# Optimization experiments

Measured on AMD Instinct MI355X. Metric: run time of the kernel, lower is better.

Reference implementation:

```python
import jax, jax.numpy as jnp
import numpy as np

TEMP = 0.05  # Trainer temp


def setup_inputs() -> dict:
    key = jax.random.key(0)
    k1, k2, k3 = jax.random.split(key, 3)
    B, C, D = 4096, 32768, 256
    x = jax.random.normal(k1, (B, D), dtype=jnp.float32)
    centrals = jax.random.normal(k2, (C, D), dtype=jnp.float32)
    # memory bank rows are kept unit-norm by the update rule
    centrals = centrals / jnp.linalg.norm(centrals, axis=1, keepdims=True)
    labels = jax.random.randint(k3, (B,), 0, C)
    return {"x": x, "centrals": centrals, "labels": labels}


def reference(x, centrals, labels):
    # new_f = F.normalize(model_out, dim=1)
    f = x / jnp.linalg.norm(x, axis=1, keepdims=True)          # [B, D]
    # CM.forward: inputs.mm(features.t()), then /= temp
    logits = (f @ centrals.T) / TEMP                           # [B, C]
    # ups = gather(exp(logits), labels); down = sum(exp(logits));  ups/down == softmax prob at label
    logp = jax.nn.log_softmax(logits, axis=1)
    p = jnp.exp(jnp.take_along_axis(logp, labels[:, None], axis=1)[:, 0])  # [B]
    return p
```

## Files before the change

kernel.cpp:

```cpp
#include <hip/hip_runtime.h>
#include <stdint.h>

typedef int i32x4 __attribute__((ext_vector_type(4)));
typedef int i32x8 __attribute__((ext_vector_type(8)));
typedef float f32x4 __attribute__((ext_vector_type(4)));

#define B_ROWS 4096
#define C_COLS 32768
#define D_DIM 256
#define LOG2E_OVER_TEMP 28.853900817779268f

#define BM 256
#define BC 128
#define CSPLIT 64
#define CPB (C_COLS / CSPLIT)
#define CTILES (CPB / BC)
#define NWAVES 4
#define TILE_BYTES (BC * D_DIM)
#define CVT_TILES (C_COLS / BC)

typedef __attribute__((address_space(3))) char lds_char_t;
typedef __attribute__((address_space(1))) const char glb_char_t;

__device__ __forceinline__ int pack4_fp8(float a, float b, float c, float d) {
  int r = 0;
  r = __builtin_amdgcn_cvt_pk_fp8_f32(a, b, r, false);
  r = __builtin_amdgcn_cvt_pk_fp8_f32(c, d, r, true);
  return r;
}

__global__ void prep_all(const float* __restrict__ x, const float* __restrict__ cent,
                         const int* __restrict__ labels, uint8_t* __restrict__ cq,
                         uint8_t* __restrict__ xq, float* __restrict__ elab) {
  int blk = blockIdx.x;
  if (blk < CVT_TILES) {
    int ct = blk;
    const float* tsrc = cent + (size_t)ct * BC * D_DIM;
    uint8_t* tdst = cq + (size_t)ct * TILE_BYTES;
    #pragma unroll
    for (int i = 0; i < 8; i++) {
      int c = i * 256 + threadIdx.x;
      int col = c >> 4;
      int k16 = c & 15;
      const float* src = tsrc + c * 16;
      int4 o;
      float4 v;
      v = ((const float4*)src)[0]; o.x = pack4_fp8(v.x, v.y, v.z, v.w);
      v = ((const float4*)src)[1]; o.y = pack4_fp8(v.x, v.y, v.z, v.w);
      v = ((const float4*)src)[2]; o.z = pack4_fp8(v.x, v.y, v.z, v.w);
      v = ((const float4*)src)[3]; o.w = pack4_fp8(v.x, v.y, v.z, v.w);
      int off = (k16 >> 1) * 4096 + (k16 & 1) * 2048 + col * 16;
      *(int4*)(tdst + off) = o;
    }
  } else {
    int row = (blk - CVT_TILES) * (blockDim.x >> 6) + (threadIdx.x >> 6);
    int lane = threadIdx.x & 63;
    int lab = labels[row];
    const float4 xv = *(const float4*)(x + (size_t)row * D_DIM + lane * 4);
    const float4 cv = *(const float4*)(cent + (size_t)lab * D_DIM + lane * 4);
    float ss = xv.x * xv.x + xv.y * xv.y + xv.z * xv.z + xv.w * xv.w;
    float dc = xv.x * cv.x + xv.y * cv.y + xv.z * cv.z + xv.w * cv.w;
    #pragma unroll
    for (int m = 1; m < 64; m <<= 1) {
      ss += __shfl_xor(ss, m, 64);
      dc += __shfl_xor(dc, m, 64);
    }
    float inv = 1.0f / sqrtf(ss);
    float sc = inv * LOG2E_OVER_TEMP;
    *(int*)(xq + (size_t)row * D_DIM + lane * 4) =
        pack4_fp8(xv.x * sc, xv.y * sc, xv.z * sc, xv.w * sc);
    if (lane == 0) elab[row] = exp2f(dc * inv * LOG2E_OVER_TEMP);
  }
}

__device__ __forceinline__ void stage_tile(const uint8_t* __restrict__ src, char* buf,
                                           int w, int lane) {
  #pragma unroll
  for (int i = 0; i < 8; i++) {
    int slot_hi = i * NWAVES + w;
    __builtin_amdgcn_global_load_lds(
        (glb_char_t*)(const void*)(src + slot_hi * 1024 + lane * 16),
        (lds_char_t*)(void*)(buf + slot_hi * 1024), 16, 0, 0);
  }
}

__global__ void __launch_bounds__(256, 2)
gemm_expsum(const uint8_t* __restrict__ xq, const uint8_t* __restrict__ cq,
            float* __restrict__ partials) {
  __shared__ char Bs[2][TILE_BYTES];
  const int tid = threadIdx.x;
  const int w = tid >> 6, lane = tid & 63;
  const int fr = lane & 15, kq = lane >> 4;

  const int bid = blockIdx.x;
  const int xcd = bid & 7;
  const int j = bid >> 3;
  const int bx = j & 15;
  const int cs = xcd * 8 + (j >> 4);
  const int brow0 = bx * BM;
  const int tile0 = cs * CTILES;

  i32x8 a[4][2];
  #pragma unroll
  for (int rf = 0; rf < 4; rf++) {
    int row = brow0 + w * 64 + rf * 16 + fr;
    #pragma unroll
    for (int kh = 0; kh < 2; kh++)
      a[rf][kh] = *(const i32x8*)(xq + (size_t)row * D_DIM + kh * 128 + kq * 32);
  }

  float s[4][4] = {{0.f,0.f,0.f,0.f},{0.f,0.f,0.f,0.f},{0.f,0.f,0.f,0.f},{0.f,0.f,0.f,0.f}};
  const f32x4 vzero = {0.f, 0.f, 0.f, 0.f};

  stage_tile(cq + (size_t)tile0 * TILE_BYTES, Bs[0], w, lane);

  for (int t = 0; t < CTILES; t++) {
    __syncthreads();
    if (t + 1 < CTILES)
      stage_tile(cq + (size_t)(tile0 + t + 1) * TILE_BYTES, Bs[(t + 1) & 1], w, lane);

    const char* buf = Bs[t & 1];
    #pragma unroll
    for (int cf = 0; cf < 8; cf++) {
      const int col = cf * 16 + fr;
      i32x8 bf[2];
      #pragma unroll
      for (int kh = 0; kh < 2; kh++) {
        const int kb = kh * 4 + kq;
        const int off = kb * 4096 + col * 16;
        i32x4 lo = *(const i32x4*)(buf + off);
        i32x4 hi = *(const i32x4*)(buf + off + 2048);
        i32x8 b;
        #pragma unroll
        for (int q = 0; q < 4; q++) { b[q] = lo[q]; b[q + 4] = hi[q]; }
        bf[kh] = b;
      }
      f32x4 acc[4];
      #pragma unroll
      for (int rf = 0; rf < 4; rf++) {
        acc[rf] = __builtin_amdgcn_mfma_scale_f32_16x16x128_f8f6f4(
            a[rf][0], bf[0], vzero, 0, 0, 0, 0x7F7F7F7F, 0, 0x7F7F7F7F);
        acc[rf] = __builtin_amdgcn_mfma_scale_f32_16x16x128_f8f6f4(
            a[rf][1], bf[1], acc[rf], 0, 0, 0, 0x7F7F7F7F, 0, 0x7F7F7F7F);
      }
      #pragma unroll
      for (int rf = 0; rf < 4; rf++)
        #pragma unroll
        for (int r = 0; r < 4; r++)
          s[rf][r] += __builtin_amdgcn_exp2f(acc[rf][r]);
    }
  }

  #pragma unroll
  for (int rf = 0; rf < 4; rf++)
    #pragma unroll
    for (int r = 0; r < 4; r++) {
      float v = s[rf][r];
      v += __shfl_xor(v, 1, 64);
      v += __shfl_xor(v, 2, 64);
      v += __shfl_xor(v, 4, 64);
      v += __shfl_xor(v, 8, 64);
      s[rf][r] = v;
    }
  if (fr == 0) {
    int rowbase = brow0 + w * 64;
    #pragma unroll
    for (int rf = 0; rf < 4; rf++)
      #pragma unroll
      for (int r = 0; r < 4; r++)
        partials[(size_t)cs * B_ROWS + rowbase + rf * 16 + kq * 4 + r] = s[rf][r];
  }
}

__global__ void finalize(const float* __restrict__ partials, const float* __restrict__ elab,
                         float* __restrict__ out) {
  int b = blockIdx.x * blockDim.x + threadIdx.x;
  if (b >= B_ROWS) return;
  float ssum = 0.f;
  #pragma unroll
  for (int cs = 0; cs < CSPLIT; cs++) ssum += partials[(size_t)cs * B_ROWS + b];
  out[b] = elab[b] / ssum;
}

extern "C" void kernel_launch(void* const* d_in, const int* in_sizes, int n_in,
                              void* d_out, int out_size, void* d_ws, size_t ws_size,
                              hipStream_t stream) {
  const float* x = (const float*)d_in[0];
  const float* cent = (const float*)d_in[1];
  const int* labels = (const int*)d_in[2];
  float* out = (float*)d_out;

  char* ws = (char*)d_ws;
  uint8_t* xq = (uint8_t*)ws;
  uint8_t* cq = (uint8_t*)(ws + (size_t)B_ROWS * D_DIM);
  float* partials = (float*)(ws + (size_t)B_ROWS * D_DIM + (size_t)C_COLS * D_DIM);
  float* elab = partials + (size_t)CSPLIT * B_ROWS;

  prep_all<<<CVT_TILES + B_ROWS / 4, 256, 0, stream>>>(x, cent, labels, cq, xq, elab);
  gemm_expsum<<<dim3(B_ROWS / BM * CSPLIT), 256, 0, stream>>>(xq, cq, partials);
  finalize<<<B_ROWS / 256, 256, 0, stream>>>(partials, elab, out);
}
```

Baseline: 67.75 us.

## Give each wave a private double-buffered B tile and drop block barriers

Shrinks the centroid tile to 32 columns and has each wave stage its own copy into a private double-buffered LDS slot. Explicit vmcnt waits replace the per-tile __syncthreads. The goal is to remove block-wide synchronization stalls between the four waves. In exchange, every wave fetches the same B data, so global/L2 traffic for the centroid matrix rises about fourfold and there are many more, smaller tiles.

```diff
diff --git a/kernel.cpp b/kernel.cpp
--- a/kernel.cpp
+++ b/kernel.cpp
@@ -11,10 +11,10 @@
 #define LOG2E_OVER_TEMP 28.853900817779268f
 
 #define BM 256
-#define BC 128
+#define BC 32
 #define CSPLIT 64
 #define CPB (C_COLS / CSPLIT)
-#define CTILES (CPB / BC)
+#define NTILES (CPB / BC)
 #define NWAVES 4
 #define TILE_BYTES (BC * D_DIM)
 #define CVT_TILES (C_COLS / BC)
@@ -38,7 +38,7 @@
     const float* tsrc = cent + (size_t)ct * BC * D_DIM;
     uint8_t* tdst = cq + (size_t)ct * TILE_BYTES;
     #pragma unroll
-    for (int i = 0; i < 8; i++) {
+    for (int i = 0; i < 2; i++) {
       int c = i * 256 + threadIdx.x;
       int col = c >> 4;
       int k16 = c & 15;
@@ -49,7 +49,7 @@
       v = ((const float4*)src)[1]; o.y = pack4_fp8(v.x, v.y, v.z, v.w);
       v = ((const float4*)src)[2]; o.z = pack4_fp8(v.x, v.y, v.z, v.w);
       v = ((const float4*)src)[3]; o.w = pack4_fp8(v.x, v.y, v.z, v.w);
-      int off = (k16 >> 1) * 4096 + (k16 & 1) * 2048 + col * 16;
+      int off = (k16 >> 1) * 1024 + (k16 & 1) * 512 + col * 16;
       *(int4*)(tdst + off) = o;
     }
   } else {
@@ -73,21 +73,20 @@
   }
 }
 
-__device__ __forceinline__ void stage_tile(const uint8_t* __restrict__ src, char* buf,
-                                           int w, int lane) {
+__device__ __forceinline__ void stage_tile_wave(const uint8_t* __restrict__ src,
+                                                char* buf, int lane) {
   #pragma unroll
   for (int i = 0; i < 8; i++) {
-    int slot_hi = i * NWAVES + w;
     __builtin_amdgcn_global_load_lds(
-        (glb_char_t*)(const void*)(src + slot_hi * 1024 + lane * 16),
-        (lds_char_t*)(void*)(buf + slot_hi * 1024), 16, 0, 0);
+        (glb_char_t*)(const void*)(src + i * 1024 + lane * 16),
+        (lds_char_t*)(void*)(buf + i * 1024), 16, 0, 0);
   }
 }
 
 __global__ void __launch_bounds__(256, 2)
 gemm_expsum(const uint8_t* __restrict__ xq, const uint8_t* __restrict__ cq,
             float* __restrict__ partials) {
-  __shared__ char Bs[2][TILE_BYTES];
+  __shared__ char Bs[NWAVES][2][TILE_BYTES];
   const int tid = threadIdx.x;
   const int w = tid >> 6, lane = tid & 63;
   const int fr = lane & 15, kq = lane >> 4;
@@ -98,7 +97,7 @@
   const int bx = j & 15;
   const int cs = xcd * 8 + (j >> 4);
   const int brow0 = bx * BM;
-  const int tile0 = cs * CTILES;
+  const int tile0 = cs * NTILES;
 
   i32x8 a[4][2];
   #pragma unroll
@@ -112,24 +111,29 @@
   float s[4][4] = {{0.f,0.f,0.f,0.f},{0.f,0.f,0.f,0.f},{0.f,0.f,0.f,0.f},{0.f,0.f,0.f,0.f}};
   const f32x4 vzero = {0.f, 0.f, 0.f, 0.f};
 
-  stage_tile(cq + (size_t)tile0 * TILE_BYTES, Bs[0], w, lane);
-
-  for (int t = 0; t < CTILES; t++) {
-    __syncthreads();
-    if (t + 1 < CTILES)
-      stage_tile(cq + (size_t)(tile0 + t + 1) * TILE_BYTES, Bs[(t + 1) & 1], w, lane);
-
-    const char* buf = Bs[t & 1];
-    #pragma unroll
-    for (int cf = 0; cf < 8; cf++) {
+  const uint8_t* csrc = cq + (size_t)tile0 * TILE_BYTES;
+  stage_tile_wave(csrc, Bs[w][0], lane);
+
+  for (int t = 0; t < NTILES; t++) {
+    if (t + 1 < NTILES) {
+      stage_tile_wave(csrc + (size_t)(t + 1) * TILE_BYTES, Bs[w][(t + 1) & 1], lane);
+      asm volatile("s_waitcnt vmcnt(8)" ::: "memory");
+    } else {
+      asm volatile("s_waitcnt vmcnt(0)" ::: "memory");
+    }
+    __builtin_amdgcn_sched_barrier(0);
+
+    const char* buf = Bs[w][t & 1];
+    #pragma unroll
+    for (int cf = 0; cf < 2; cf++) {
       const int col = cf * 16 + fr;
       i32x8 bf[2];
       #pragma unroll
       for (int kh = 0; kh < 2; kh++) {
         const int kb = kh * 4 + kq;
-        const int off = kb * 4096 + col * 16;
+        const int off = kb * 1024 + col * 16;
         i32x4 lo = *(const i32x4*)(buf + off);
-        i32x4 hi = *(const i32x4*)(buf + off + 2048);
+        i32x4 hi = *(const i32x4*)(buf + off + 512);
         i32x8 b;
         #pragma unroll
         for (int q = 0; q < 4; q++) { b[q] = lo[q]; b[q + 4] = hi[q]; }
```

Result: slower. 71.87 us (+6.1%).
